# Kernel optimization log

Measured on AMD Instinct MI355X. Metric: run time of the kernel, lower is better.

Reference implementation:

```python
import jax, jax.numpy as jnp
import numpy as np

D_MODEL = 1024
D_STATE = 16
D_CONV = 4
EXPAND = 2
D_INNER = D_MODEL * EXPAND
B = 1
L = 2048


def setup_inputs() -> dict:
    key = jax.random.key(0)
    ks = jax.random.split(key, 8)
    s = lambda k, shape, scale: jax.random.normal(k, shape, dtype=jnp.float32) * scale
    return {
        "x": jax.random.normal(ks[0], (B, L, D_MODEL), dtype=jnp.float32),
        "in_proj_w": s(ks[1], (D_INNER * 2, D_MODEL), D_MODEL ** -0.5),
        "conv_w": s(ks[2], (D_INNER, 1, D_CONV), D_CONV ** -0.5),  # depthwise [O, I/g=1, K]
        "conv_b": jnp.zeros((D_INNER,), jnp.float32),
        "x_proj_w": s(ks[3], (2 * D_STATE + 1, D_INNER), D_INNER ** -0.5),
        "dt_proj_w": s(ks[4], (D_INNER, 1), 1.0),
        "dt_proj_b": jnp.zeros((D_INNER,), jnp.float32),
        "A_log": jnp.log(jnp.broadcast_to(jnp.arange(1, D_STATE + 1, dtype=jnp.float32), (D_INNER, D_STATE))),
        "D": jnp.ones((D_INNER,), jnp.float32),
        "out_proj_w": s(ks[5], (D_MODEL, D_INNER), D_INNER ** -0.5),
    }


def reference(x, in_proj_w, conv_w, conv_b, x_proj_w, dt_proj_w, dt_proj_b, A_log, D, out_proj_w):
    Bb = x.shape[0]
    # in_proj -> split into ssm branch and gate z
    xz = x @ in_proj_w.T                      # [B, L, 2*Di]
    x_ssm, z = jnp.split(xz, 2, axis=-1)
    # causal depthwise conv1d (torch pads K-1 both sides then slices [:L] == left-pad K-1)
    xt = jnp.swapaxes(x_ssm, 1, 2)            # [B, Di, L]
    xc = jax.lax.conv_general_dilated(
        xt, conv_w, window_strides=(1,), padding=[(D_CONV - 1, 0)],
        feature_group_count=D_INNER, dimension_numbers=("NCH", "OIH", "NCH"))
    xc = xc + conv_b[None, :, None]
    xc = jax.nn.silu(jnp.swapaxes(xc, 1, 2))  # [B, L, Di]
    # selective SSM
    A = -jnp.exp(A_log)                        # [Di, N]
    xp = xc @ x_proj_w.T                       # [B, L, 1+2N]
    dt_r = xp[..., :1]
    Bv = xp[..., 1:1 + D_STATE]                # [B, L, N]
    Cv = xp[..., 1 + D_STATE:]                 # [B, L, N]
    dt = jax.nn.softplus(dt_r @ dt_proj_w.T + dt_proj_b)   # [B, L, Di]
    dA = jnp.exp(dt[..., None] * A)                          # [B, L, Di, N]
    dBx = dt[..., None] * Bv[:, :, None, :] * xc[..., None]  # [B, L, Di, N]

    def step(h, inps):
        dA_t, dBx_t, C_t = inps
        h = dA_t * h + dBx_t                   # [B, Di, N]
        y = jnp.einsum("bdn,bn->bd", h, C_t)
        return h, y

    h0 = jnp.zeros((Bb, D_INNER, D_STATE), x.dtype)
    _, ys = jax.lax.scan(step, h0, (jnp.swapaxes(dA, 0, 1), jnp.swapaxes(dBx, 0, 1), jnp.swapaxes(Cv, 0, 1)))
    y = jnp.swapaxes(ys, 0, 1) + xc * D        # [B, L, Di]
    return (y * jax.nn.silu(z)) @ out_proj_w.T
```

## Files before the change

kernel.cpp:

```cpp
#include <hip/hip_runtime.h>
#include <math.h>

#define L_SEQ   2048
#define DM      1024
#define DI      2048
#define NST     16
#define LC      32
#define NCHUNK  64
#define XP_LD   36
#define KSPLIT  8
#define LOG2E   1.44269504f

typedef short s16x8 __attribute__((ext_vector_type(8)));
typedef float f32x4 __attribute__((ext_vector_type(4)));

__device__ __forceinline__ float silu_f(float x) {
  return x / (1.0f + __expf(-x));
}
__device__ __forceinline__ float softplus_f(float x) {
  return x > 20.0f ? x : __logf(1.0f + __expf(x));
}
__device__ __forceinline__ ushort f2bf(float f) {
  unsigned int u = __float_as_uint(f);
  unsigned int r = (u + 0x7fffu + ((u >> 16) & 1u)) >> 16;
  return (ushort)r;
}
__device__ __forceinline__ void gload_lds16(const void* g, void* lds) {
  __builtin_amdgcn_global_load_lds(
      (const __attribute__((address_space(1))) unsigned int*)g,
      (__attribute__((address_space(3))) unsigned int*)lds,
      16, 0, 0);
}

__global__ __launch_bounds__(256) void cvt_bf16_k(
    const float* __restrict__ in, ushort* __restrict__ out, int n4) {
  int i = blockIdx.x * 256 + threadIdx.x;
  if (i >= n4) return;
  float4 v = ((const float4*)in)[i];
  ushort4 o;
  o.x = f2bf(v.x); o.y = f2bf(v.y); o.z = f2bf(v.z); o.w = f2bf(v.w);
  ((ushort4*)out)[i] = o;
}

template <int MFRAG>
__global__ __launch_bounds__(256) void gemm_mfma_bf16(
    const ushort* __restrict__ A, const ushort* __restrict__ B,
    float* __restrict__ C, int K, int ldc) {
  constexpr int BM = MFRAG * 32;
  __shared__ ushort As[BM * 32];
  __shared__ ushort Bs[128 * 32];
  const int tid  = threadIdx.x;
  const int lane = tid & 63;
  const int wv   = tid >> 6;
  const int wr   = wv >> 1;
  const int wc   = wv & 1;
  const int m0 = blockIdx.y * BM;
  const int n0 = blockIdx.x * 128;

  f32x4 acc[MFRAG][4] = {};

  const int kc = (tid & 3) * 8;

  for (int k0 = 0; k0 < K; k0 += 32) {
    __syncthreads();
#pragma unroll
    for (int q = 0; q < BM / 64; ++q) {
      int id = q * 256 + tid;
      int m  = id >> 2;
      gload_lds16(A + (size_t)(m0 + m) * K + k0 + kc, (char*)As + id * 16);
    }
#pragma unroll
    for (int q = 0; q < 2; ++q) {
      int id = q * 256 + tid;
      int n  = id >> 2;
      gload_lds16(B + (size_t)(n0 + n) * K + k0 + kc, (char*)Bs + id * 16);
    }
    __syncthreads();

    s16x8 af[MFRAG], bfr[4];
#pragma unroll
    for (int m = 0; m < MFRAG; ++m)
      af[m] = *(const s16x8*)&As[(wr * MFRAG * 16 + m * 16 + (lane & 15)) * 32 + (lane >> 4) * 8];
#pragma unroll
    for (int n = 0; n < 4; ++n)
      bfr[n] = *(const s16x8*)&Bs[(wc * 64 + n * 16 + (lane & 15)) * 32 + (lane >> 4) * 8];
#pragma unroll
    for (int m = 0; m < MFRAG; ++m)
#pragma unroll
      for (int n = 0; n < 4; ++n)
        acc[m][n] = __builtin_amdgcn_mfma_f32_16x16x32_bf16(af[m], bfr[n], acc[m][n], 0, 0, 0);
  }
  const int cr = (lane >> 4) * 4;
  const int cc = lane & 15;
#pragma unroll
  for (int m = 0; m < MFRAG; ++m) {
    int gr0 = m0 + wr * MFRAG * 16 + m * 16 + cr;
#pragma unroll
    for (int n = 0; n < 4; ++n) {
      int gc = n0 + wc * 64 + n * 16 + cc;
#pragma unroll
      for (int r = 0; r < 4; ++r)
        C[(size_t)(gr0 + r) * ldc + gc] = acc[m][n][r];
    }
  }
}

__global__ __launch_bounds__(256) void conv_silu_k(
    const float* __restrict__ xz, const float* __restrict__ cw,
    const float* __restrict__ cb, float* __restrict__ xc) {
  const int d = blockIdx.x * 256 + threadIdx.x;
  const int l = blockIdx.y;
  const float w0 = cw[d*4+0], w1 = cw[d*4+1], w2 = cw[d*4+2], w3 = cw[d*4+3];
  float acc = cb[d];
  if (l >= 3) acc = fmaf(w0, xz[(size_t)(l-3)*4096 + d], acc);
  if (l >= 2) acc = fmaf(w1, xz[(size_t)(l-2)*4096 + d], acc);
  if (l >= 1) acc = fmaf(w2, xz[(size_t)(l-1)*4096 + d], acc);
  acc = fmaf(w3, xz[(size_t)l*4096 + d], acc);
  xc[(size_t)l*DI + d] = silu_f(acc);
}

__global__ __launch_bounds__(256) void transpose_k(
    const float* __restrict__ in, float* __restrict__ out) {
  __shared__ float tile[64][65];
  const int d0 = blockIdx.x * 64, l0 = blockIdx.y * 64;
  const int r  = threadIdx.x >> 4;
  const int c4 = (threadIdx.x & 15) * 4;
#pragma unroll
  for (int p = 0; p < 4; ++p) {
    float4 v = *(const float4*)&in[(size_t)(l0 + r + p*16) * DI + d0 + c4];
    tile[r + p*16][c4+0] = v.x; tile[r + p*16][c4+1] = v.y;
    tile[r + p*16][c4+2] = v.z; tile[r + p*16][c4+3] = v.w;
  }
  __syncthreads();
  const int dd = threadIdx.x >> 4;
  const int l4 = (threadIdx.x & 15) * 4;
#pragma unroll
  for (int p = 0; p < 4; ++p) {
    float4 v;
    v.x = tile[l4+0][dd + p*16];
    v.y = tile[l4+1][dd + p*16];
    v.z = tile[l4+2][dd + p*16];
    v.w = tile[l4+3][dd + p*16];
    *(float4*)&out[(size_t)(d0 + dd + p*16) * L_SEQ + l0 + l4] = v;
  }
}

__global__ __launch_bounds__(256) void gemm_xp_k(
    const float* __restrict__ xc, const float* __restrict__ Wxp,
    float* __restrict__ xp_part) {
  const int L0   = blockIdx.x * 64;
  const int ks   = blockIdx.y;
  const int wv   = threadIdx.x >> 6;
  const int lane = threadIdx.x & 63;
  __shared__ float xcs[64][65];
  __shared__ float Ws[36][64];
  float acc[9] = {};
  const int kbeg = ks * (DI / KSPLIT);
  const int kend = kbeg + DI / KSPLIT;
  for (int k0 = kbeg; k0 < kend; k0 += 64) {
    {
      int r = threadIdx.x >> 2;
      int cbase = (threadIdx.x & 3) * 16;
#pragma unroll
      for (int q = 0; q < 4; ++q) {
        float4 v = *(const float4*)&xc[(size_t)(L0 + r) * DI + k0 + cbase + q*4];
        xcs[r][cbase + q*4 + 0] = v.x; xcs[r][cbase + q*4 + 1] = v.y;
        xcs[r][cbase + q*4 + 2] = v.z; xcs[r][cbase + q*4 + 3] = v.w;
      }
    }
    for (int idx = threadIdx.x; idx < 36 * 16; idx += 256) {
      int j = idx >> 4; int cc = (idx & 15) << 2;
      float4 v = make_float4(0.f, 0.f, 0.f, 0.f);
      if (j < 33) v = *(const float4*)&Wxp[(size_t)j * DI + k0 + cc];
      *(float4*)&Ws[j][cc] = v;
    }
    __syncthreads();
#pragma unroll 4
    for (int kk = 0; kk < 64; kk += 4) {
      float4 wr[9];
#pragma unroll
      for (int jj = 0; jj < 9; ++jj) wr[jj] = *(const float4*)&Ws[wv*9 + jj][kk];
      float a0 = xcs[lane][kk+0], a1 = xcs[lane][kk+1];
      float a2 = xcs[lane][kk+2], a3 = xcs[lane][kk+3];
#pragma unroll
      for (int jj = 0; jj < 9; ++jj) {
        acc[jj] = fmaf(a0, wr[jj].x, acc[jj]);
        acc[jj] = fmaf(a1, wr[jj].y, acc[jj]);
        acc[jj] = fmaf(a2, wr[jj].z, acc[jj]);
        acc[jj] = fmaf(a3, wr[jj].w, acc[jj]);
      }
    }
    __syncthreads();
  }
  const int l = L0 + lane;
#pragma unroll
  for (int jj = 0; jj < 9; ++jj) {
    int j = wv * 9 + jj;
    if (j < 33)
      xp_part[(size_t)ks * L_SEQ * XP_LD + (size_t)l * XP_LD + j] = acc[jj];
  }
}

__global__ __launch_bounds__(256) void reduce_xp_k(
    const float* __restrict__ part, float* __restrict__ xp) {
  int i = blockIdx.x * 256 + threadIdx.x;
  float s = 0.f;
#pragma unroll
  for (int ks = 0; ks < KSPLIT; ++ks)
    s += part[(size_t)ks * L_SEQ * XP_LD + i];
  xp[i] = s;
}

__device__ __forceinline__ void stage_xps(
    float (*xps)[36], const float* __restrict__ xp, int l0, int tid) {
  for (int idx = tid; idx < LC * 33; idx += 256) {
    int rr = idx / 33, j = idx - rr * 33;
    int col = (j == 0) ? 32 : j - 1;
    xps[rr][col] = xp[(size_t)(l0 + rr) * XP_LD + j];
  }
}

__device__ __forceinline__ void stage_xcs(
    float (*xcs)[LC + 1], const float* __restrict__ xcT, int d0, int l0, int tid) {
#pragma unroll
  for (int q = 0; q < 4; ++q) {
    int f4  = q * 256 + tid;
    int row = f4 >> 3;
    int col = (f4 & 7) * 4;
    float4 v = *(const float4*)&xcT[(size_t)(d0 + row) * L_SEQ + l0 + col];
    xcs[row][col+0] = v.x; xcs[row][col+1] = v.y;
    xcs[row][col+2] = v.z; xcs[row][col+3] = v.w;
  }
}

__global__ __launch_bounds__(256) void scan_partial_k(
    const float* __restrict__ xcT, const float* __restrict__ xp,
    const float* __restrict__ dtw, const float* __restrict__ dtb,
    const float* __restrict__ A_log,
    float* __restrict__ P, float* __restrict__ Q) {
  const int tid = threadIdx.x;
  const int dl  = tid >> 1;
  const int d0  = blockIdx.x * 128;
  const int d   = d0 + dl;
  const int nb  = (tid & 1) * 8;
  const int c   = blockIdx.y;
  const int l0  = c * LC;
  __shared__ float xps[LC][36];
  __shared__ float xcs[128][LC + 1];
  stage_xps(xps, xp, l0, tid);
  stage_xcs(xcs, xcT, d0, l0, tid);

  float Ad2[8];
#pragma unroll
  for (int j4 = 0; j4 < 8; j4 += 4) {
    float4 v = *(const float4*)&A_log[(size_t)d * NST + nb + j4];
    Ad2[j4+0] = -__expf(v.x) * LOG2E; Ad2[j4+1] = -__expf(v.y) * LOG2E;
    Ad2[j4+2] = -__expf(v.z) * LOG2E; Ad2[j4+3] = -__expf(v.w) * LOG2E;
  }
  const float w = dtw[d], b = dtb[d];
  float h[8];
#pragma unroll
  for (int n = 0; n < 8; ++n) h[n] = 0.f;
  float sumdt = 0.f;
  __syncthreads();
#pragma unroll 4
  for (int t = 0; t < LC; ++t) {
    float dt  = softplus_f(fmaf(xps[t][32], w, b));
    sumdt += dt;
    float dtx = dt * xcs[dl][t];
    f32x4 B0 = *(const f32x4*)&xps[t][nb];
    f32x4 B1 = *(const f32x4*)&xps[t][nb + 4];
    float Bv[8];
    *(f32x4*)&Bv[0] = B0; *(f32x4*)&Bv[4] = B1;
#pragma unroll
    for (int n = 0; n < 8; ++n) {
      float da = exp2f(dt * Ad2[n]);
      h[n] = fmaf(da, h[n], dtx * Bv[n]);
    }
  }
  float p[8];
#pragma unroll
  for (int n = 0; n < 8; ++n) p[n] = exp2f(sumdt * Ad2[n]);
  size_t base = ((size_t)c * DI + d) * NST + nb;
  *(float4*)&P[base]     = make_float4(p[0], p[1], p[2], p[3]);
  *(float4*)&P[base + 4] = make_float4(p[4], p[5], p[6], p[7]);
  *(float4*)&Q[base]     = make_float4(h[0], h[1], h[2], h[3]);
  *(float4*)&Q[base + 4] = make_float4(h[4], h[5], h[6], h[7]);
}

__global__ __launch_bounds__(256) void scan_prefix_k(
    const float* __restrict__ P, float* __restrict__ QHs) {
  const int g = blockIdx.x * 256 + threadIdx.x;
  const int d = g >> 2;
  const int q = (g & 3) << 2;
  float4 h = make_float4(0.f, 0.f, 0.f, 0.f);
#pragma unroll 8
  for (int c = 0; c < NCHUNK; ++c) {
    size_t base = ((size_t)c * DI + d) * NST + q;
    float4 pv = *(const float4*)&P[base];
    float4 qv = *(const float4*)&QHs[base];
    *(float4*)&QHs[base] = h;
    h.x = fmaf(pv.x, h.x, qv.x);
    h.y = fmaf(pv.y, h.y, qv.y);
    h.z = fmaf(pv.z, h.z, qv.z);
    h.w = fmaf(pv.w, h.w, qv.w);
  }
}

__global__ __launch_bounds__(256) void scan_final_k(
    const float* __restrict__ xcT, const float* __restrict__ xp,
    const float* __restrict__ dtw, const float* __restrict__ dtb,
    const float* __restrict__ A_log, const float* __restrict__ Dp,
    const float* __restrict__ Hs, const float* __restrict__ xz,
    ushort* __restrict__ ys) {
  const int tid  = threadIdx.x;
  const int dl   = tid >> 1;
  const int d0   = blockIdx.x * 128;
  const int d    = d0 + dl;
  const int half = tid & 1;
  const int nb   = half * 8;
  const int c    = blockIdx.y;
  const int l0   = c * LC;
  __shared__ float xps[LC][36];
  __shared__ float xcs[128][LC + 1];
  __shared__ float zs[LC][128];
#pragma unroll
  for (int q = 0; q < 4; ++q) {
    int id = q * 256 + tid;
    int t  = id >> 5;
    int c4 = (id & 31) * 4;
    gload_lds16(xz + (size_t)(l0 + t) * 4096 + 2048 + d0 + c4,
                (char*)zs + id * 16);
  }
  stage_xps(xps, xp, l0, tid);
  stage_xcs(xcs, xcT, d0, l0, tid);

  float Ad2[8];
#pragma unroll
  for (int j4 = 0; j4 < 8; j4 += 4) {
    float4 v = *(const float4*)&A_log[(size_t)d * NST + nb + j4];
    Ad2[j4+0] = -__expf(v.x) * LOG2E; Ad2[j4+1] = -__expf(v.y) * LOG2E;
    Ad2[j4+2] = -__expf(v.z) * LOG2E; Ad2[j4+3] = -__expf(v.w) * LOG2E;
  }
  const float w = dtw[d], b = dtb[d], Dd = Dp[d];
  float h[8];
  size_t hb = ((size_t)c * DI + d) * NST + nb;
  *(float4*)&h[0] = *(const float4*)&Hs[hb];
  *(float4*)&h[4] = *(const float4*)&Hs[hb + 4];
  __syncthreads();
#pragma unroll 4
  for (int t = 0; t < LC; ++t) {
    const int l = l0 + t;
    float dt  = softplus_f(fmaf(xps[t][32], w, b));
    float xcv = xcs[dl][t];
    float dtx = dt * xcv;
    f32x4 B0 = *(const f32x4*)&xps[t][nb];
    f32x4 B1 = *(const f32x4*)&xps[t][nb + 4];
    f32x4 C0 = *(const f32x4*)&xps[t][16 + nb];
    f32x4 C1 = *(const f32x4*)&xps[t][20 + nb];
    float Bv[8], Cv[8];
    *(f32x4*)&Bv[0] = B0; *(f32x4*)&Bv[4] = B1;
    *(f32x4*)&Cv[0] = C0; *(f32x4*)&Cv[4] = C1;
    float y = 0.f;
#pragma unroll
    for (int n = 0; n < 8; ++n) {
      float da = exp2f(dt * Ad2[n]);
      h[n] = fmaf(da, h[n], dtx * Bv[n]);
      y = fmaf(h[n], Cv[n], y);
    }
    y += __shfl_xor(y, 1);
    if (half == 0) {
      y = fmaf(xcv, Dd, y);
      ys[(size_t)l * DI + d] = f2bf(y * silu_f(zs[t][dl]));
    }
  }
}

extern "C" void kernel_launch(void* const* d_in, const int* in_sizes, int n_in,
                              void* d_out, int out_size, void* d_ws, size_t ws_size,
                              hipStream_t stream) {
  const float* x    = (const float*)d_in[0];
  const float* W1   = (const float*)d_in[1];
  const float* cw   = (const float*)d_in[2];
  const float* cb   = (const float*)d_in[3];
  const float* Wxp  = (const float*)d_in[4];
  const float* dtw  = (const float*)d_in[5];
  const float* dtb  = (const float*)d_in[6];
  const float* Alog = (const float*)d_in[7];
  const float* Dp   = (const float*)d_in[8];
  const float* Wout = (const float*)d_in[9];
  float* out = (float*)d_out;

  char* w = (char*)d_ws;
  float*  xz      = (float*)w;
  float*  xcT     = (float*)(w + 33554432);
  float*  xc_rm   = (float*)(w + 50331648);
  ushort* x_bf    = (ushort*)(w + 50331648);
  ushort* W1_bf   = (ushort*)(w + 54525952);
  float*  P       = (float*)(w + 50331648);
  float*  QHs     = (float*)(w + 58720256);
  float*  xp      = (float*)(w + 67108864);
  ushort* Wout_bf = (ushort*)(w + 67403776);
  ushort* ys_bf   = (ushort*)(w + 71598080);
  float*  xp_part = (float*)(w + 71598080);

  cvt_bf16_k<<<2048, 256, 0, stream>>>(x,    x_bf,    2048*1024/4);
  cvt_bf16_k<<<4096, 256, 0, stream>>>(W1,   W1_bf,   4096*1024/4);
  cvt_bf16_k<<<2048, 256, 0, stream>>>(Wout, Wout_bf, 1024*2048/4);
  gemm_mfma_bf16<4><<<dim3(4096/128, 2048/128), 256, 0, stream>>>(x_bf, W1_bf, xz, DM, 4096);
  conv_silu_k<<<dim3(DI/256, L_SEQ), 256, 0, stream>>>(xz, cw, cb, xc_rm);
  transpose_k<<<dim3(DI/64, L_SEQ/64), 256, 0, stream>>>(xc_rm, xcT);
  gemm_xp_k<<<dim3(L_SEQ/64, KSPLIT), 256, 0, stream>>>(xc_rm, Wxp, xp_part);
  reduce_xp_k<<<L_SEQ*XP_LD/256, 256, 0, stream>>>(xp_part, xp);
  scan_partial_k<<<dim3(DI/128, NCHUNK), 256, 0, stream>>>(xcT, xp, dtw, dtb, Alog, P, QHs);
  scan_prefix_k<<<DI*NST/4/256, 256, 0, stream>>>(P, QHs);
  scan_final_k<<<dim3(DI/128, NCHUNK), 256, 0, stream>>>(xcT, xp, dtw, dtb, Alog, Dp, QHs, xz, ys_bf);
  gemm_mfma_bf16<2><<<dim3(1024/128, 2048/64), 256, 0, stream>>>(ys_bf, Wout_bf, out, DI, 1024);
}
```

Measured before the change: 278.8 us.

## Store xz in bf16, fuse conv+silu with transpose, precompute dt in LDS

The in_proj GEMM now writes xz as bf16, which halves its store and later read traffic. The conv+silu kernel reads the bf16 tile, computes, and writes the transposed xcT directly, so the row-major xc buffer and the separate transpose kernel go away. gemm_xp now reads xcT and transposes it through LDS. Both scan kernels precompute softplus(dt) once per (t,d) into shared memory instead of redundantly in each half-lane pair. The cost is extra bf16 rounding of the x_ssm and z activations, plus added LDS use and an extra barrier in the scans.

```diff
diff --git a/kernel.cpp b/kernel.cpp
--- a/kernel.cpp
+++ b/kernel.cpp
@@ -12,6 +12,7 @@
 #define LOG2E   1.44269504f
 
 typedef short s16x8 __attribute__((ext_vector_type(8)));
+typedef unsigned short u16x8 __attribute__((ext_vector_type(8)));
 typedef float f32x4 __attribute__((ext_vector_type(4)));
 
 __device__ __forceinline__ float silu_f(float x) {
@@ -24,6 +25,9 @@
   unsigned int u = __float_as_uint(f);
   unsigned int r = (u + 0x7fffu + ((u >> 16) & 1u)) >> 16;
   return (ushort)r;
+}
+__device__ __forceinline__ float bf2f(ushort u) {
+  return __uint_as_float((unsigned int)u << 16);
 }
 __device__ __forceinline__ void gload_lds16(const void* g, void* lds) {
   __builtin_amdgcn_global_load_lds(
@@ -42,10 +46,10 @@
   ((ushort4*)out)[i] = o;
 }
 
-template <int MFRAG>
+template <int MFRAG, bool BF16OUT>
 __global__ __launch_bounds__(256) void gemm_mfma_bf16(
     const ushort* __restrict__ A, const ushort* __restrict__ B,
-    float* __restrict__ C, int K, int ldc) {
+    void* __restrict__ Cv, int K, int ldc) {
   constexpr int BM = MFRAG * 32;
   __shared__ ushort As[BM * 32];
   __shared__ ushort Bs[128 * 32];
@@ -58,7 +62,6 @@
   const int n0 = blockIdx.x * 128;
 
   f32x4 acc[MFRAG][4] = {};
-
   const int kc = (tid & 3) * 8;
 
   for (int k0 = 0; k0 < K; k0 += 32) {
@@ -99,54 +102,64 @@
     for (int n = 0; n < 4; ++n) {
       int gc = n0 + wc * 64 + n * 16 + cc;
 #pragma unroll
-      for (int r = 0; r < 4; ++r)
-        C[(size_t)(gr0 + r) * ldc + gc] = acc[m][n][r];
-    }
-  }
-}
-
-__global__ __launch_bounds__(256) void conv_silu_k(
-    const float* __restrict__ xz, const float* __restrict__ cw,
-    const float* __restrict__ cb, float* __restrict__ xc) {
-  const int d = blockIdx.x * 256 + threadIdx.x;
-  const int l = blockIdx.y;
+      for (int r = 0; r < 4; ++r) {
+        if constexpr (BF16OUT)
+          ((ushort*)Cv)[(size_t)(gr0 + r) * ldc + gc] = f2bf(acc[m][n][r]);
+        else
+          ((float*)Cv)[(size_t)(gr0 + r) * ldc + gc] = acc[m][n][r];
+      }
+    }
+  }
+}
+
+__global__ __launch_bounds__(256) void conv_silu_T_k(
+    const ushort* __restrict__ xzb, const float* __restrict__ cw,
+    const float* __restrict__ cb, float* __restrict__ xcT) {
+  const int d0  = blockIdx.x * 64;
+  const int l0  = blockIdx.y * 64;
+  const int tid = threadIdx.x;
+  __shared__ ushort xt[67][64];
+  __shared__ float  ot[64][65];
+#pragma unroll
+  for (int q = 0; q < 3; ++q) {
+    int id = q * 256 + tid;
+    if (id < 67 * 8) {
+      int row = id >> 3, c8 = (id & 7) * 8;
+      int l = l0 - 3 + row;
+      u16x8 v = (u16x8)(ushort)0;
+      if (l >= 0)
+        v = *(const u16x8*)&xzb[(size_t)l * 4096 + d0 + c8];
+      *(u16x8*)&xt[row][c8] = v;
+    }
+  }
+  __syncthreads();
+  const int dloc = tid & 63;
+  const int d    = d0 + dloc;
   const float w0 = cw[d*4+0], w1 = cw[d*4+1], w2 = cw[d*4+2], w3 = cw[d*4+3];
-  float acc = cb[d];
-  if (l >= 3) acc = fmaf(w0, xz[(size_t)(l-3)*4096 + d], acc);
-  if (l >= 2) acc = fmaf(w1, xz[(size_t)(l-2)*4096 + d], acc);
-  if (l >= 1) acc = fmaf(w2, xz[(size_t)(l-1)*4096 + d], acc);
-  acc = fmaf(w3, xz[(size_t)l*4096 + d], acc);
-  xc[(size_t)l*DI + d] = silu_f(acc);
-}
-
-__global__ __launch_bounds__(256) void transpose_k(
-    const float* __restrict__ in, float* __restrict__ out) {
-  __shared__ float tile[64][65];
-  const int d0 = blockIdx.x * 64, l0 = blockIdx.y * 64;
-  const int r  = threadIdx.x >> 4;
-  const int c4 = (threadIdx.x & 15) * 4;
-#pragma unroll
-  for (int p = 0; p < 4; ++p) {
-    float4 v = *(const float4*)&in[(size_t)(l0 + r + p*16) * DI + d0 + c4];
-    tile[r + p*16][c4+0] = v.x; tile[r + p*16][c4+1] = v.y;
-    tile[r + p*16][c4+2] = v.z; tile[r + p*16][c4+3] = v.w;
-  }
-  __syncthreads();
-  const int dd = threadIdx.x >> 4;
-  const int l4 = (threadIdx.x & 15) * 4;
-#pragma unroll
-  for (int p = 0; p < 4; ++p) {
-    float4 v;
-    v.x = tile[l4+0][dd + p*16];
-    v.y = tile[l4+1][dd + p*16];
-    v.z = tile[l4+2][dd + p*16];
-    v.w = tile[l4+3][dd + p*16];
-    *(float4*)&out[(size_t)(d0 + dd + p*16) * L_SEQ + l0 + l4] = v;
+  const float bb = cb[d];
+  const int lb = (tid >> 6) * 16;
+#pragma unroll
+  for (int j = 0; j < 16; ++j) {
+    int ll = lb + j;
+    float a = bb;
+    a = fmaf(w0, bf2f(xt[ll+0][dloc]), a);
+    a = fmaf(w1, bf2f(xt[ll+1][dloc]), a);
+    a = fmaf(w2, bf2f(xt[ll+2][dloc]), a);
+    a = fmaf(w3, bf2f(xt[ll+3][dloc]), a);
+    ot[dloc][ll] = silu_f(a);
+  }
+  __syncthreads();
+#pragma unroll
+  for (int q = 0; q < 4; ++q) {
+    int f4 = q * 256 + tid;
+    int dr = f4 >> 4, lc = (f4 & 15) * 4;
+    float4 v = make_float4(ot[dr][lc], ot[dr][lc+1], ot[dr][lc+2], ot[dr][lc+3]);
+    *(float4*)&xcT[(size_t)(d0 + dr) * L_SEQ + l0 + lc] = v;
   }
 }
 
 __global__ __launch_bounds__(256) void gemm_xp_k(
-    const float* __restrict__ xc, const float* __restrict__ Wxp,
+    const float* __restrict__ xcT, const float* __restrict__ Wxp,
     float* __restrict__ xp_part) {
   const int L0   = blockIdx.x * 64;
   const int ks   = blockIdx.y;
@@ -158,15 +171,14 @@
   const int kbeg = ks * (DI / KSPLIT);
   const int kend = kbeg + DI / KSPLIT;
   for (int k0 = kbeg; k0 < kend; k0 += 64) {
-    {
-      int r = threadIdx.x >> 2;
-      int cbase = (threadIdx.x & 3) * 16;
-#pragma unroll
-      for (int q = 0; q < 4; ++q) {
-        float4 v = *(const float4*)&xc[(size_t)(L0 + r) * DI + k0 + cbase + q*4];
-        xcs[r][cbase + q*4 + 0] = v.x; xcs[r][cbase + q*4 + 1] = v.y;
-        xcs[r][cbase + q*4 + 2] = v.z; xcs[r][cbase + q*4 + 3] = v.w;
-      }
+#pragma unroll
+    for (int q = 0; q < 4; ++q) {
+      int f4 = q * 256 + threadIdx.x;
+      int dr = f4 >> 4;
+      int lc = (f4 & 15) * 4;
+      float4 v = *(const float4*)&xcT[(size_t)(k0 + dr) * L_SEQ + L0 + lc];
+      xcs[lc+0][dr] = v.x; xcs[lc+1][dr] = v.y;
+      xcs[lc+2][dr] = v.z; xcs[lc+3][dr] = v.w;
     }
     for (int idx = threadIdx.x; idx < 36 * 16; idx += 256) {
       int j = idx >> 4; int cc = (idx & 15) << 2;
@@ -219,7 +231,6 @@
     xps[rr][col] = xp[(size_t)(l0 + rr) * XP_LD + j];
   }
 }
-
 __device__ __forceinline__ void stage_xcs(
     float (*xcs)[LC + 1], const float* __restrict__ xcT, int d0, int l0, int tid) {
 #pragma unroll
@@ -231,6 +242,17 @@
     xcs[row][col+0] = v.x; xcs[row][col+1] = v.y;
     xcs[row][col+2] = v.z; xcs[row][col+3] = v.w;
   }
+}
+__device__ __forceinline__ void stage_dts(
+    float (*dts)[128], float (*xps)[36],
+    const float* __restrict__ dtw, const float* __restrict__ dtb,
+    int d0, int tid) {
+  int dd = tid & 127;
+  int tb = (tid >> 7) * 16;
+  float wv = dtw[d0 + dd], bv = dtb[d0 + dd];
+#pragma unroll
+  for (int j = 0; j < 16; ++j)
+    dts[tb + j][dd] = softplus_f(fmaf(xps[tb + j][32], wv, bv));
 }
 
 __global__ __launch_bounds__(256) void scan_partial_k(
@@ -247,6 +269,7 @@
   const int l0  = c * LC;
   __shared__ float xps[LC][36];
   __shared__ float xcs[128][LC + 1];
+  __shared__ float dts[LC][128];
   stage_xps(xps, xp, l0, tid);
   stage_xcs(xcs, xcT, d0, l0, tid);
 
@@ -257,7 +280,8 @@
     Ad2[j4+0] = -__expf(v.x) * LOG2E; Ad2[j4+1] = -__expf(v.y) * LOG2E;
     Ad2[j4+2] = -__expf(v.z) * LOG2E; Ad2[j4+3] = -__expf(v.w) * LOG2E;
   }
-  const float w = dtw[d], b = dtb[d];
+  __syncthreads();
+  stage_dts(dts, xps, dtw, dtb, d0, tid);
   float h[8];
 #pragma unroll
   for (int n = 0; n < 8; ++n) h[n] = 0.f;
@@ -265,7 +289,7 @@
   __syncthreads();
 #pragma unroll 4
   for (int t = 0; t < LC; ++t) {
-    float dt  = softplus_f(fmaf(xps[t][32], w, b));
+    float dt  = dts[t][dl];
     sumdt += dt;
     float dtx = dt * xcs[dl][t];
     f32x4 B0 = *(const f32x4*)&xps[t][nb];
@@ -311,7 +335,7 @@
     const float* __restrict__ xcT, const float* __restrict__ xp,
     const float* __restrict__ dtw, const float* __restrict__ dtb,
     const float* __restrict__ A_log, const float* __restrict__ Dp,
-    const float* __restrict__ Hs, const float* __restrict__ xz,
+    const float* __restrict__ Hs, const ushort* __restrict__ xzb,
     ushort* __restrict__ ys) {
   const int tid  = threadIdx.x;
   const int dl   = tid >> 1;
@@ -321,15 +345,16 @@
   const int nb   = half * 8;
   const int c    = blockIdx.y;
   const int l0   = c * LC;
-  __shared__ float xps[LC][36];
-  __shared__ float xcs[128][LC + 1];
-  __shared__ float zs[LC][128];
-#pragma unroll
-  for (int q = 0; q < 4; ++q) {
+  __shared__ float  xps[LC][36];
+  __shared__ float  xcs[128][LC + 1];
+  __shared__ float  dts[LC][128];
+  __shared__ ushort zs[LC][128];
+#pragma unroll
+  for (int q = 0; q < 2; ++q) {
     int id = q * 256 + tid;
-    int t  = id >> 5;
-    int c4 = (id & 31) * 4;
-    gload_lds16(xz + (size_t)(l0 + t) * 4096 + 2048 + d0 + c4,
+    int t  = id >> 4;
+    int c8 = (id & 15) * 8;
+    gload_lds16(xzb + (size_t)(l0 + t) * 4096 + 2048 + d0 + c8,
                 (char*)zs + id * 16);
   }
   stage_xps(xps, xp, l0, tid);
@@ -342,16 +367,18 @@
     Ad2[j4+0] = -__expf(v.x) * LOG2E; Ad2[j4+1] = -__expf(v.y) * LOG2E;
     Ad2[j4+2] = -__expf(v.z) * LOG2E; Ad2[j4+3] = -__expf(v.w) * LOG2E;
   }
-  const float w = dtw[d], b = dtb[d], Dd = Dp[d];
+  const float Dd = Dp[d];
   float h[8];
   size_t hb = ((size_t)c * DI + d) * NST + nb;
   *(float4*)&h[0] = *(const float4*)&Hs[hb];
   *(float4*)&h[4] = *(const float4*)&Hs[hb + 4];
   __syncthreads();
+  stage_dts(dts, xps, dtw, dtb, d0, tid);
+  __syncthreads();
 #pragma unroll 4
   for (int t = 0; t < LC; ++t) {
     const int l = l0 + t;
-    float dt  = softplus_f(fmaf(xps[t][32], w, b));
+    float dt  = dts[t][dl];
     float xcv = xcs[dl][t];
     float dtx = dt * xcv;
     f32x4 B0 = *(const f32x4*)&xps[t][nb];
@@ -371,7 +398,7 @@
     y += __shfl_xor(y, 1);
     if (half == 0) {
       y = fmaf(xcv, Dd, y);
-      ys[(size_t)l * DI + d] = f2bf(y * silu_f(zs[t][dl]));
+      ys[(size_t)l * DI + d] = f2bf(y * silu_f(bf2f(zs[t][dl])));
     }
   }
 }
@@ -392,28 +419,28 @@
   float* out = (float*)d_out;
 
   char* w = (char*)d_ws;
-  float*  xz      = (float*)w;
-  float*  xcT     = (float*)(w + 33554432);
-  float*  xc_rm   = (float*)(w + 50331648);
-  ushort* x_bf    = (ushort*)(w + 50331648);
-  ushort* W1_bf   = (ushort*)(w + 54525952);
-  float*  P       = (float*)(w + 50331648);
-  float*  QHs     = (float*)(w + 58720256);
-  float*  xp      = (float*)(w + 67108864);
-  ushort* Wout_bf = (ushort*)(w + 67403776);
-  ushort* ys_bf   = (ushort*)(w + 71598080);
-  float*  xp_part = (float*)(w + 71598080);
+  ushort* xz_bf   = (ushort*)w;
+  float*  xcT     = (float*)(w + 16777216);
+  ushort* x_bf    = (ushort*)(w + 33554432);
+  ushort* W1_bf   = (ushort*)(w + 37748736);
+  float*  P       = (float*)(w + 33554432);
+  float*  QHs     = (float*)(w + 41943040);
+  float*  xp      = (float*)(w + 50331648);
+  ushort* Wout_bf = (ushort*)(w + 50626560);
+  ushort* ys_bf   = (ushort*)(w + 54820864);
+  float*  xp_part = (float*)(w + 54820864);
 
   cvt_bf16_k<<<2048, 256, 0, stream>>>(x,    x_bf,    2048*1024/4);
   cvt_bf16_k<<<4096, 256, 0, stream>>>(W1,   W1_bf,   4096*1024/4);
   cvt_bf16_k<<<2048, 256, 0, stream>>>(Wout, Wout_bf, 1024*2048/4);
-  gemm_mfma_bf16<4><<<dim3(4096/128, 2048/128), 256, 0, stream>>>(x_bf, W1_bf, xz, DM, 4096);
-  conv_silu_k<<<dim3(DI/256, L_SEQ), 256, 0, stream>>>(xz, cw, cb, xc_rm);
-  transpose_k<<<dim3(DI/64, L_SEQ/64), 256, 0, stream>>>(xc_rm, xcT);
-  gemm_xp_k<<<dim3(L_SEQ/64, KSPLIT), 256, 0, stream>>>(xc_rm, Wxp, xp_part);
+  gemm_mfma_bf16<4, true><<<dim3(4096/128, 2048/128), 256, 0, stream>>>(
+      x_bf, W1_bf, xz_bf, DM, 4096);
+  conv_silu_T_k<<<dim3(DI/64, L_SEQ/64), 256, 0, stream>>>(xz_bf, cw, cb, xcT);
+  gemm_xp_k<<<dim3(L_SEQ/64, KSPLIT), 256, 0, stream>>>(xcT, Wxp, xp_part);
   reduce_xp_k<<<L_SEQ*XP_LD/256, 256, 0, stream>>>(xp_part, xp);
   scan_partial_k<<<dim3(DI/128, NCHUNK), 256, 0, stream>>>(xcT, xp, dtw, dtb, Alog, P, QHs);
   scan_prefix_k<<<DI*NST/4/256, 256, 0, stream>>>(P, QHs);
-  scan_final_k<<<dim3(DI/128, NCHUNK), 256, 0, stream>>>(xcT, xp, dtw, dtb, Alog, Dp, QHs, xz, ys_bf);
-  gemm_mfma_bf16<2><<<dim3(1024/128, 2048/64), 256, 0, stream>>>(ys_bf, Wout_bf, out, DI, 1024);
-}
+  scan_final_k<<<dim3(DI/128, NCHUNK), 256, 0, stream>>>(xcT, xp, dtw, dtb, Alog, Dp, QHs, xz_bf, ys_bf);
+  gemm_mfma_bf16<2, false><<<dim3(1024/128, 2048/64), 256, 0, stream>>>(
+      ys_bf, Wout_bf, out, DI, 1024);
+}
```

After: 264.9 us. -5.0%, faster.
